# Kernel optimization log

Hardware: AMD Instinct MI355X
Metric: run time of the kernel (lower is better)

## Reference

```python
import jax, jax.numpy as jnp
import numpy as np

B, P, D = 8, 576, 1024
H = 16
HD = D // H  # 64
HID = 4 * D  # 4096
EPS = 1e-6  # flax LayerNorm default


def _ln(x, g, b):
    m = jnp.mean(x, axis=-1, keepdims=True)
    v = jnp.var(x, axis=-1, keepdims=True)
    return (x - m) * jax.lax.rsqrt(v + EPS) * g + b


def setup_inputs() -> dict:
    key = jax.random.key(0)
    ks = jax.random.split(key, 8)
    s = 0.02
    return {
        "x": jax.random.normal(ks[0], (B, P, D), dtype=jnp.float32),
        "w_qkv": jax.random.normal(ks[1], (D, 3 * D), dtype=jnp.float32) * s,
        "q_g": jnp.ones((HD,), jnp.float32), "q_b": jnp.zeros((HD,), jnp.float32),
        "k_g": jnp.ones((HD,), jnp.float32), "k_b": jnp.zeros((HD,), jnp.float32),
        "o_g": jnp.ones((D,), jnp.float32), "o_b": jnp.zeros((D,), jnp.float32),
        "w_proj": jax.random.normal(ks[2], (D, D), dtype=jnp.float32) * s,
        "b_proj": jnp.zeros((D,), jnp.float32),
        "ln1_g": jnp.ones((D,), jnp.float32), "ln1_b": jnp.zeros((D,), jnp.float32),
        "ln2_g": jnp.ones((D,), jnp.float32), "ln2_b": jnp.zeros((D,), jnp.float32),
        "w1": jax.random.normal(ks[3], (D, HID), dtype=jnp.float32) * s,
        "b1": jnp.zeros((HID,), jnp.float32),
        "w2": jax.random.normal(ks[4], (HID, D), dtype=jnp.float32) * s,
        "b2": jnp.zeros((D,), jnp.float32),
        "ls1": jnp.full((D,), 1e-5, jnp.float32),
        "ls2": jnp.full((D,), 1e-5, jnp.float32),
    }


def reference(x, w_qkv, q_g, q_b, k_g, k_b, o_g, o_b, w_proj, b_proj,
              ln1_g, ln1_b, ln2_g, ln2_b, w1, b1, w2, b2, ls1, ls2):
    scale = HD ** (-0.5)
    # --- attention branch ---
    o = _ln(x, ln1_g, ln1_b)
    qkv = jnp.einsum('bpd,de->bpe', o, w_qkv)
    qkv = qkv.reshape(B, P, 3, H, HD).transpose(2, 0, 3, 1, 4)  # [3,B,H,P,HD]
    q, k, v = qkv[0], qkv[1], qkv[2]
    q = _ln(q, q_g, q_b) * scale  # QK-LayerNorm per head
    k = _ln(k, k_g, k_b)
    attn = jax.nn.softmax(jnp.einsum('bhqd,bhkd->bhqk', q, k), axis=-1)
    o = jnp.einsum('bhqk,bhkd->bhqd', attn, v)
    o = jnp.swapaxes(o, 1, 2).reshape(B, P, D)
    o = _ln(o, o_g, o_b)
    o = jnp.einsum('bpd,de->bpe', o, w_proj) + b_proj
    x = x + o * ls1
    # --- MLP branch ---
    o = _ln(x, ln2_g, ln2_b)
    o = jax.nn.gelu(jnp.einsum('bpd,dh->bph', o, w1) + b1)  # tanh-approx gelu (flax default)
    o = jnp.einsum('bph,hd->bpd', o, w2) + b2
    return x + o * ls2
```

## Files before the change

kernel.cpp:

```cpp
#include <hip/hip_runtime.h>
#include <hip/hip_bf16.h>

#define DEV static __device__ __forceinline__

typedef short frag8 __attribute__((ext_vector_type(8)));
typedef float accf4 __attribute__((ext_vector_type(4)));


DEV unsigned short f2bf(float f){
  union { float f; unsigned int u; } v; v.f = f;
  unsigned int r = v.u + 0x7fffu + ((v.u >> 16) & 1u);
  return (unsigned short)(r >> 16);
}

DEV void gload16(const void* g, void* l){
  __builtin_amdgcn_global_load_lds((const __attribute__((address_space(1))) void*)g,
                                   (__attribute__((address_space(3))) void*)l, 16, 0, 0);
}

DEV float gelu_tanh(float x){
  float u = 0.7978845608028654f * (x + 0.044715f * x * x * x);
  float e = __expf(2.0f * u);
  float th = 1.0f - 2.0f / (e + 1.0f);
  return 0.5f * x * (1.0f + th);
}

DEV void block_map(int bid, int nwg, int gx, int& tx, int& ty){
  const int swz = ((nwg & 7) == 0) ? ((bid & 7) * (nwg >> 3) + (bid >> 3)) : bid;
  const int gy = nwg / gx;
  const int cg = swz / (gy * 16);
  const int rr = swz - cg * gy * 16;
  const int gw = min(16, gx - cg * 16);
  tx = cg * 16 + rr % gw;
  ty = rr / gw;
}

__global__ __launch_bounds__(256) void wtrans(const float* __restrict__ W,
                                              unsigned short* __restrict__ Wt,
                                              int K, int N){
  __shared__ float t[32][33];
  const int n0 = blockIdx.x * 32, k0 = blockIdx.y * 32;
  const int tx = threadIdx.x, ty = threadIdx.y;
  #pragma unroll
  for (int i = 0; i < 4; i++)
    t[ty + i*8][tx] = W[(long)(k0 + ty + i*8) * N + n0 + tx];
  __syncthreads();
  #pragma unroll
  for (int i = 0; i < 4; i++)
    Wt[(long)(n0 + ty + i*8) * K + k0 + tx] = f2bf(t[tx][ty + i*8]);
}

__global__ __launch_bounds__(256) void ln_rows(const float* __restrict__ in,
                                               const float* __restrict__ g,
                                               const float* __restrict__ beta,
                                               unsigned short* __restrict__ out){
  const long row = blockIdx.x;
  const int t = threadIdx.x;
  const float4 v = ((const float4*)(in + row * 1024))[t];
  float s  = v.x + v.y + v.z + v.w;
  float s2 = v.x*v.x + v.y*v.y + v.z*v.z + v.w*v.w;
  #pragma unroll
  for (int o = 32; o; o >>= 1){ s += __shfl_xor(s, o); s2 += __shfl_xor(s2, o); }
  __shared__ float rs[4], rq[4];
  const int wv = t >> 6;
  if ((t & 63) == 0){ rs[wv] = s; rq[wv] = s2; }
  __syncthreads();
  s  = rs[0] + rs[1] + rs[2] + rs[3];
  s2 = rq[0] + rq[1] + rq[2] + rq[3];
  const float mean = s * (1.f/1024.f);
  const float inv = rsqrtf(s2 * (1.f/1024.f) - mean*mean + 1e-6f);
  const float4 gv = ((const float4*)g)[t];
  const float4 bv = ((const float4*)beta)[t];
  ushort4 o4;
  o4.x = f2bf((v.x - mean)*inv*gv.x + bv.x);
  o4.y = f2bf((v.y - mean)*inv*gv.y + bv.y);
  o4.z = f2bf((v.z - mean)*inv*gv.z + bv.z);
  o4.w = f2bf((v.w - mean)*inv*gv.w + bv.w);
  *(ushort4*)(out + row * 1024 + t * 4) = o4;
}

__global__ __launch_bounds__(256) void attn_k(const unsigned short* __restrict__ Qn,
                                              const unsigned short* __restrict__ Kn,
                                              const unsigned short* __restrict__ Vt,
                                              float* __restrict__ O){
  __shared__ __align__(16) unsigned short Ks[2][4096];
  __shared__ __align__(16) unsigned short Vs[2][4096];
  __shared__ __align__(16) unsigned short Plds[4096];
  const int f = blockIdx.x;
  const int xcd = f & 7, j = f >> 3;
  const int bh = xcd * 16 + j / 9;
  const int qb = j - (j / 9) * 9;
  const int b = bh >> 4, h = bh & 15;
  const int tid = threadIdx.x, w = tid >> 6, l = tid & 63;
  const int fr = l & 15, fq = l >> 4;
  const int rsw = fr & 7;
  const int q0 = qb * 64;

  const unsigned short* qbase = Qn + ((long)bh * 576 + q0 + w * 16 + fr) * 64;
  const frag8 qf0 = *(const frag8*)(qbase + fq * 8);
  const frag8 qf1 = *(const frag8*)(qbase + 32 + fq * 8);

  const int r8 = l >> 3;
  const int kq8 = ((l & 7) ^ r8) * 8;
  const unsigned short* kSrc = Kn + ((long)bh * 576 + w * 16 + r8) * 64 + kq8;
  const unsigned short* vSrc = Vt + ((long)bh * 64 + w * 16 + r8) * 576 + kq8;

  auto stage = [&](int d, int t){
    gload16(kSrc + (long)t * 4096,              &Ks[d][w * 1024]);
    gload16(kSrc + (long)t * 4096 + 512,        &Ks[d][w * 1024 + 512]);
    gload16(vSrc + (long)t * 64,                &Vs[d][w * 1024]);
    gload16(vSrc + (long)t * 64 + 8l * 576,     &Vs[d][w * 1024 + 512]);
  };

  accf4 oacc[4];
  #pragma unroll
  for (int nd = 0; nd < 4; nd++) oacc[nd] = (accf4){0.f, 0.f, 0.f, 0.f};
  float m[4] = {-1e30f, -1e30f, -1e30f, -1e30f};
  float lsum[4] = {0.f, 0.f, 0.f, 0.f};

  stage(0, 0);
  __syncthreads();
  int cur = 0;
  for (int t = 0; t < 9; ++t){
    if (t < 8) stage(cur ^ 1, t + 1);

    accf4 st[4];
    #pragma unroll
    for (int kt4 = 0; kt4 < 4; kt4++){
      const int c0 = ((0 * 4 + fq) ^ rsw) * 8;
      const int c1 = ((1 * 4 + fq) ^ rsw) * 8;
      frag8 kf0 = *(const frag8*)&Ks[cur][(kt4 * 16 + fr) * 64 + c0];
      frag8 kf1 = *(const frag8*)&Ks[cur][(kt4 * 16 + fr) * 64 + c1];
      accf4 a = {0.f, 0.f, 0.f, 0.f};
      a = __builtin_amdgcn_mfma_f32_16x16x32_bf16(qf0, kf0, a, 0, 0, 0);
      a = __builtin_amdgcn_mfma_f32_16x16x32_bf16(qf1, kf1, a, 0, 0, 0);
      st[kt4] = a;
    }

    #pragma unroll
    for (int rr = 0; rr < 4; rr++){
      float v = fmaxf(fmaxf(st[0][rr], st[1][rr]), fmaxf(st[2][rr], st[3][rr]));
      #pragma unroll
      for (int o = 8; o; o >>= 1) v = fmaxf(v, __shfl_xor(v, o));
      const float mn = fmaxf(m[rr], v);
      const float sc = __expf(m[rr] - mn);
      float p[4], rs = 0.f;
      #pragma unroll
      for (int kt4 = 0; kt4 < 4; kt4++){ p[kt4] = __expf(st[kt4][rr] - mn); rs += p[kt4]; }
      #pragma unroll
      for (int o = 8; o; o >>= 1) rs += __shfl_xor(rs, o);
      lsum[rr] = lsum[rr] * sc + rs;
      m[rr] = mn;
      #pragma unroll
      for (int nd = 0; nd < 4; nd++) oacc[nd][rr] *= sc;
      const int prow = fq * 4 + rr;
      #pragma unroll
      for (int kt4 = 0; kt4 < 4; kt4++){
        const int chunk = kt4 * 2 + (fr >> 3);
        Plds[w * 1024 + prow * 64 + ((chunk ^ (prow & 7)) << 3) + (fr & 7)] = f2bf(p[kt4]);
      }
    }

    #pragma unroll
    for (int nd = 0; nd < 4; nd++){
      const int c0 = ((0 * 4 + fq) ^ rsw) * 8;
      const int c1 = ((1 * 4 + fq) ^ rsw) * 8;
      frag8 af0 = *(const frag8*)&Plds[w * 1024 + fr * 64 + c0];
      frag8 af1 = *(const frag8*)&Plds[w * 1024 + fr * 64 + c1];
      frag8 vf0 = *(const frag8*)&Vs[cur][(nd * 16 + fr) * 64 + c0];
      frag8 vf1 = *(const frag8*)&Vs[cur][(nd * 16 + fr) * 64 + c1];
      oacc[nd] = __builtin_amdgcn_mfma_f32_16x16x32_bf16(af0, vf0, oacc[nd], 0, 0, 0);
      oacc[nd] = __builtin_amdgcn_mfma_f32_16x16x32_bf16(af1, vf1, oacc[nd], 0, 0, 0);
    }

    __syncthreads();
    cur ^= 1;
  }

  #pragma unroll
  for (int rr = 0; rr < 4; rr++){
    const float rinv = 1.f / lsum[rr];
    const long orow = (long)b * 576 + q0 + w * 16 + fq * 4 + rr;
    #pragma unroll
    for (int nd = 0; nd < 4; nd++)
      O[orow * 1024 + h * 64 + nd * 16 + fr] = oacc[nd][rr] * rinv;
  }
}

template<int BN, int EPI>
__global__ __launch_bounds__(256) void gemm_bk64(
    const unsigned short* __restrict__ A, const unsigned short* __restrict__ Bt,
    float* __restrict__ Cf, unsigned short* __restrict__ Cb,
    const float* __restrict__ bias, const float* __restrict__ ls,
    const float* __restrict__ resid,
    const float* __restrict__ qg, const float* __restrict__ qb2,
    const float* __restrict__ kg, const float* __restrict__ kb2,
    unsigned short* __restrict__ Qn, unsigned short* __restrict__ Kn,
    unsigned short* __restrict__ Vt,
    int M, int N, int K, int gx)
{
  constexpr int NF = BN / 32;
  constexpr int BSLOT = BN / 32;
  __shared__ __align__(16) unsigned short As[2][128 * 64];
  __shared__ __align__(16) unsigned short Bs[2][BN * 64];
  const int tid = threadIdx.x;
  const int wave = tid >> 6, l = tid & 63;
  const int fr = l & 15, fq = l >> 4;
  const int wr = wave >> 1, wc = wave & 1;
  const int rsw = fr & 7;
  int tx, ty;
  block_map(blockIdx.x, gridDim.x, gx, tx, ty);
  const long rowbase = (long)ty * 128;
  const long colbase = (long)tx * BN;

  const int r8 = l >> 3;
  const int kq = (l & 7) ^ r8;
  const unsigned short* aS = A + (rowbase + wave*32 + r8) * (long)K + kq * 8;
  const unsigned short* bS = Bt + (colbase + wave*(BN/4) + r8) * (long)K + kq * 8;

  accf4 acc[4][NF];
  const accf4 zero = {0.f, 0.f, 0.f, 0.f};
  #pragma unroll
  for (int m = 0; m < 4; m++)
    #pragma unroll
    for (int n = 0; n < NF; n++) acc[m][n] = zero;

  auto stage = [&](int d, int t){
    const long k0 = (long)t * 64;
    #pragma unroll
    for (int s = 0; s < 4; s++)
      gload16(aS + (long)s * 8 * K + k0, &As[d][(wave*4 + s) * 512]);
    #pragma unroll
    for (int s = 0; s < BSLOT; s++)
      gload16(bS + (long)s * 8 * K + k0, &Bs[d][(wave*BSLOT + s) * 512]);
  };
  auto compute = [&](int d){
    #pragma unroll
    for (int kk = 0; kk < 2; kk++){
      const int csw = ((kk * 4 + fq) ^ rsw) * 8;
      frag8 bf[NF];
      #pragma unroll
      for (int n = 0; n < NF; n++)
        bf[n] = *(const frag8*)&Bs[d][(wc*(BN/2) + n*16 + fr) * 64 + csw];
      #pragma unroll
      for (int m = 0; m < 4; m++){
        frag8 af = *(const frag8*)&As[d][(wr*64 + m*16 + fr) * 64 + csw];
        #pragma unroll
        for (int n = 0; n < NF; n++)
          acc[m][n] = __builtin_amdgcn_mfma_f32_16x16x32_bf16(af, bf[n], acc[m][n], 0, 0, 0);
      }
    }
  };

  const int NT = K >> 6;
  stage(0, 0);
  __syncthreads();
  int cur = 0;
  for (int t = 0; t < NT; ++t){
    if (t + 1 < NT) stage(cur ^ 1, t + 1);
    compute(cur);
    __syncthreads();
    cur ^= 1;
  }

  if constexpr (EPI == 3){
    const int cg = (int)colbase + wc * 64;
    const int kind = cg >> 10;
    const int h = (cg & 1023) >> 6;
    if (kind < 2){
      const float* g  = kind ? kg : qg;
      const float* bb = kind ? kb2 : qb2;
      const float sc = kind ? 1.0f : 0.125f;
      unsigned short* Out = kind ? Kn : Qn;
      #pragma unroll
      for (int m = 0; m < 4; m++){
        #pragma unroll
        for (int r = 0; r < 4; r++){
          float s1 = 0.f, s2 = 0.f;
          #pragma unroll
          for (int n = 0; n < NF; n++){ const float v = acc[m][n][r]; s1 += v; s2 += v*v; }
          #pragma unroll
          for (int o = 8; o; o >>= 1){ s1 += __shfl_xor(s1, o); s2 += __shfl_xor(s2, o); }
          const float mean = s1 * (1.f/64.f);
          const float inv = rsqrtf(s2 * (1.f/64.f) - mean*mean + 1e-6f);
          const long row = rowbase + wr*64 + m*16 + fq*4 + r;
          const int bq = (int)(row / 576), p = (int)(row - (long)bq*576);
          unsigned short* dst = Out + (((long)(bq*16 + h))*576 + p)*64;
          #pragma unroll
          for (int n = 0; n < NF; n++){
            const int d = n*16 + fr;
            dst[d] = f2bf(((acc[m][n][r] - mean)*inv*g[d] + bb[d]) * sc);
          }
        }
      }
    } else {
      #pragma unroll
      for (int m = 0; m < 4; m++){
        const long grow = rowbase + wr*64 + m*16 + fq*4;
        const int bq = (int)(grow / 576), p = (int)(grow - (long)bq*576);
        #pragma unroll
        for (int n = 0; n < NF; n++){
          const int d = n*16 + fr;
          ushort4 o4;
          o4.x = f2bf(acc[m][n][0]); o4.y = f2bf(acc[m][n][1]);
          o4.z = f2bf(acc[m][n][2]); o4.w = f2bf(acc[m][n][3]);
          *(ushort4*)(Vt + ((long)(bq*16 + h)*64 + d)*576 + p) = o4;
        }
      }
    }
  } else {
    #pragma unroll
    for (int m = 0; m < 4; m++){
      const long rb = rowbase + wr * 64 + m * 16 + fq * 4;
      #pragma unroll
      for (int n = 0; n < NF; n++){
        const long cb = colbase + wc * (BN/2) + n * 16 + fr;
        #pragma unroll
        for (int r = 0; r < 4; r++){
          const long idx = (rb + r) * N + cb;
          const float v = acc[m][n][r];
          if constexpr (EPI == 1){
            Cf[idx] = resid[idx] + (v + bias[cb]) * ls[cb];
          } else {
            Cb[idx] = f2bf(gelu_tanh(v + bias[cb]));
          }
        }
      }
    }
  }
}

extern "C" void kernel_launch(void* const* d_in, const int* in_sizes, int n_in,
                              void* d_out, int out_size, void* d_ws, size_t ws_size,
                              hipStream_t stream){
  (void)in_sizes; (void)n_in; (void)out_size; (void)ws_size;
  const float* x      = (const float*)d_in[0];
  const float* w_qkv  = (const float*)d_in[1];
  const float* q_g    = (const float*)d_in[2];
  const float* q_b    = (const float*)d_in[3];
  const float* k_g    = (const float*)d_in[4];
  const float* k_b    = (const float*)d_in[5];
  const float* o_g    = (const float*)d_in[6];
  const float* o_b    = (const float*)d_in[7];
  const float* w_proj = (const float*)d_in[8];
  const float* b_proj = (const float*)d_in[9];
  const float* ln1_g  = (const float*)d_in[10];
  const float* ln1_b  = (const float*)d_in[11];
  const float* ln2_g  = (const float*)d_in[12];
  const float* ln2_b  = (const float*)d_in[13];
  const float* w1     = (const float*)d_in[14];
  const float* b1     = (const float*)d_in[15];
  const float* w2     = (const float*)d_in[16];
  const float* b2     = (const float*)d_in[17];
  const float* ls1    = (const float*)d_in[18];
  const float* ls2    = (const float*)d_in[19];
  float* out = (float*)d_out;

  char* ws = (char*)d_ws;
  size_t off = 0;
  auto alloc = [&](size_t bytes)->void*{
    void* p = ws + off; off += (bytes + 255) & ~(size_t)255; return p;
  };
  unsigned short* wqkvT  = (unsigned short*)alloc(3072l*1024*2);
  unsigned short* wprojT = (unsigned short*)alloc(1024l*1024*2);
  unsigned short* w1T    = (unsigned short*)alloc(4096l*1024*2);
  unsigned short* w2T    = (unsigned short*)alloc(1024l*4096*2);
  unsigned short* xnA    = (unsigned short*)alloc(4608l*1024*2);
  unsigned short* Qn     = (unsigned short*)alloc(73728l*64*2);
  unsigned short* Kn     = (unsigned short*)alloc(73728l*64*2);
  unsigned short* Vt     = (unsigned short*)alloc(73728l*64*2);
  unsigned short* hbf    = (unsigned short*)alloc(4608l*4096*2);
  float*          attnO  = (float*)alloc(4608l*1024*4);

  wtrans<<<dim3(3072/32, 1024/32), dim3(32,8), 0, stream>>>(w_qkv,  wqkvT,  1024, 3072);
  wtrans<<<dim3(1024/32, 1024/32), dim3(32,8), 0, stream>>>(w_proj, wprojT, 1024, 1024);
  wtrans<<<dim3(4096/32, 1024/32), dim3(32,8), 0, stream>>>(w1,     w1T,    1024, 4096);
  wtrans<<<dim3(1024/32, 4096/32), dim3(32,8), 0, stream>>>(w2,     w2T,    4096, 1024);

  ln_rows<<<4608, 256, 0, stream>>>(x, ln1_g, ln1_b, xnA);
  gemm_bk64<128,3><<<24*36, 256, 0, stream>>>(xnA, wqkvT, nullptr, nullptr,
                                              nullptr, nullptr, nullptr,
                                              q_g, q_b, k_g, k_b, Qn, Kn, Vt,
                                              4608, 3072, 1024, 24);
  attn_k<<<1152, 256, 0, stream>>>(Qn, Kn, Vt, attnO);
  ln_rows<<<4608, 256, 0, stream>>>(attnO, o_g, o_b, xnA);
  gemm_bk64<64,1><<<16*36, 256, 0, stream>>>(xnA, wprojT, out, nullptr,
                                             b_proj, ls1, x,
                                             nullptr, nullptr, nullptr, nullptr,
                                             nullptr, nullptr, nullptr,
                                             4608, 1024, 1024, 16);
  ln_rows<<<4608, 256, 0, stream>>>(out, ln2_g, ln2_b, xnA);
  gemm_bk64<64,2><<<64*36, 256, 0, stream>>>(xnA, w1T, nullptr, hbf,
                                             b1, nullptr, nullptr,
                                             nullptr, nullptr, nullptr, nullptr,
                                             nullptr, nullptr, nullptr,
                                             4608, 4096, 1024, 64);
  gemm_bk64<64,1><<<16*36, 256, 0, stream>>>(hbf, w2T, out, nullptr,
                                             b2, ls2, out,
                                             nullptr, nullptr, nullptr, nullptr,
                                             nullptr, nullptr, nullptr,
                                             4608, 1024, 4096, 16);
}
```

Before: 266.0 us.

## Store attention output in bf16 and split QKV GEMM into QK and V launches

The attention kernel now writes its output as bf16 instead of fp32, and the following LayerNorm reads bf16 through a templated loader, halving that intermediate's traffic. The fused QKV GEMM is split into a Q/K GEMM with the per-head LayerNorm epilogue and a separate V GEMM with BN=64 that writes the transposed V layout. This removes the divergent epilogue branch but adds a kernel launch and reloads the A operand. Rounding the attention output to bf16 before LayerNorm adds a small loss of precision.

```diff
diff --git a/kernel.cpp b/kernel.cpp
--- a/kernel.cpp
+++ b/kernel.cpp
@@ -11,6 +11,10 @@
   union { float f; unsigned int u; } v; v.f = f;
   unsigned int r = v.u + 0x7fffu + ((v.u >> 16) & 1u);
   return (unsigned short)(r >> 16);
+}
+
+DEV float bf2f(unsigned short u){
+  union { unsigned int i; float f; } v; v.i = (unsigned int)u << 16; return v.f;
 }
 
 DEV void gload16(const void* g, void* l){
@@ -50,13 +54,20 @@
     Wt[(long)(n0 + ty + i*8) * K + k0 + tx] = f2bf(t[tx][ty + i*8]);
 }
 
-__global__ __launch_bounds__(256) void ln_rows(const float* __restrict__ in,
+template<int BF>
+__global__ __launch_bounds__(256) void ln_rows(const void* __restrict__ inp,
                                                const float* __restrict__ g,
                                                const float* __restrict__ beta,
                                                unsigned short* __restrict__ out){
   const long row = blockIdx.x;
   const int t = threadIdx.x;
-  const float4 v = ((const float4*)(in + row * 1024))[t];
+  float4 v;
+  if constexpr (BF){
+    const ushort4 u = ((const ushort4*)inp)[row * 256 + t];
+    v.x = bf2f(u.x); v.y = bf2f(u.y); v.z = bf2f(u.z); v.w = bf2f(u.w);
+  } else {
+    v = ((const float4*)inp)[row * 256 + t];
+  }
   float s  = v.x + v.y + v.z + v.w;
   float s2 = v.x*v.x + v.y*v.y + v.z*v.z + v.w*v.w;
   #pragma unroll
@@ -82,7 +93,7 @@
 __global__ __launch_bounds__(256) void attn_k(const unsigned short* __restrict__ Qn,
                                               const unsigned short* __restrict__ Kn,
                                               const unsigned short* __restrict__ Vt,
-                                              float* __restrict__ O){
+                                              unsigned short* __restrict__ O){
   __shared__ __align__(16) unsigned short Ks[2][4096];
   __shared__ __align__(16) unsigned short Vs[2][4096];
   __shared__ __align__(16) unsigned short Plds[4096];
@@ -183,7 +194,7 @@
     const long orow = (long)b * 576 + q0 + w * 16 + fq * 4 + rr;
     #pragma unroll
     for (int nd = 0; nd < 4; nd++)
-      O[orow * 1024 + h * 64 + nd * 16 + fr] = oacc[nd][rr] * rinv;
+      O[orow * 1024 + h * 64 + nd * 16 + fr] = f2bf(oacc[nd][rr] * rinv);
   }
 }
 
@@ -267,45 +278,44 @@
     const int cg = (int)colbase + wc * 64;
     const int kind = cg >> 10;
     const int h = (cg & 1023) >> 6;
-    if (kind < 2){
-      const float* g  = kind ? kg : qg;
-      const float* bb = kind ? kb2 : qb2;
-      const float sc = kind ? 1.0f : 0.125f;
-      unsigned short* Out = kind ? Kn : Qn;
-      #pragma unroll
-      for (int m = 0; m < 4; m++){
+    const float* g  = kind ? kg : qg;
+    const float* bb = kind ? kb2 : qb2;
+    const float sc = kind ? 1.0f : 0.125f;
+    unsigned short* Out = kind ? Kn : Qn;
+    #pragma unroll
+    for (int m = 0; m < 4; m++){
+      #pragma unroll
+      for (int r = 0; r < 4; r++){
+        float s1 = 0.f, s2 = 0.f;
         #pragma unroll
-        for (int r = 0; r < 4; r++){
-          float s1 = 0.f, s2 = 0.f;
-          #pragma unroll
-          for (int n = 0; n < NF; n++){ const float v = acc[m][n][r]; s1 += v; s2 += v*v; }
-          #pragma unroll
-          for (int o = 8; o; o >>= 1){ s1 += __shfl_xor(s1, o); s2 += __shfl_xor(s2, o); }
-          const float mean = s1 * (1.f/64.f);
-          const float inv = rsqrtf(s2 * (1.f/64.f) - mean*mean + 1e-6f);
-          const long row = rowbase + wr*64 + m*16 + fq*4 + r;
-          const int bq = (int)(row / 576), p = (int)(row - (long)bq*576);
-          unsigned short* dst = Out + (((long)(bq*16 + h))*576 + p)*64;
-          #pragma unroll
-          for (int n = 0; n < NF; n++){
-            const int d = n*16 + fr;
-            dst[d] = f2bf(((acc[m][n][r] - mean)*inv*g[d] + bb[d]) * sc);
-          }
-        }
-      }
-    } else {
-      #pragma unroll
-      for (int m = 0; m < 4; m++){
-        const long grow = rowbase + wr*64 + m*16 + fq*4;
-        const int bq = (int)(grow / 576), p = (int)(grow - (long)bq*576);
+        for (int n = 0; n < NF; n++){ const float v = acc[m][n][r]; s1 += v; s2 += v*v; }
+        #pragma unroll
+        for (int o = 8; o; o >>= 1){ s1 += __shfl_xor(s1, o); s2 += __shfl_xor(s2, o); }
+        const float mean = s1 * (1.f/64.f);
+        const float inv = rsqrtf(s2 * (1.f/64.f) - mean*mean + 1e-6f);
+        const long row = rowbase + wr*64 + m*16 + fq*4 + r;
+        const int bq = (int)(row / 576), p = (int)(row - (long)bq*576);
+        unsigned short* dst = Out + (((long)(bq*16 + h))*576 + p)*64;
         #pragma unroll
         for (int n = 0; n < NF; n++){
           const int d = n*16 + fr;
-          ushort4 o4;
-          o4.x = f2bf(acc[m][n][0]); o4.y = f2bf(acc[m][n][1]);
-          o4.z = f2bf(acc[m][n][2]); o4.w = f2bf(acc[m][n][3]);
-          *(ushort4*)(Vt + ((long)(bq*16 + h)*64 + d)*576 + p) = o4;
+          dst[d] = f2bf(((acc[m][n][r] - mean)*inv*g[d] + bb[d]) * sc);
         }
+      }
+    }
+  } else if constexpr (EPI == 4){
+    const int h = (int)colbase >> 6;
+    #pragma unroll
+    for (int m = 0; m < 4; m++){
+      const long grow = rowbase + wr*64 + m*16 + fq*4;
+      const int bq = (int)(grow / 576), p = (int)(grow - (long)bq*576);
+      #pragma unroll
+      for (int n = 0; n < NF; n++){
+        const int d = wc*(BN/2) + n*16 + fr;
+        ushort4 o4;
+        o4.x = f2bf(acc[m][n][0]); o4.y = f2bf(acc[m][n][1]);
+        o4.z = f2bf(acc[m][n][2]); o4.w = f2bf(acc[m][n][3]);
+        *(ushort4*)(Vt + ((long)(bq*16 + h)*64 + d)*576 + p) = o4;
       }
     }
   } else {
@@ -370,26 +380,31 @@
   unsigned short* Kn     = (unsigned short*)alloc(73728l*64*2);
   unsigned short* Vt     = (unsigned short*)alloc(73728l*64*2);
   unsigned short* hbf    = (unsigned short*)alloc(4608l*4096*2);
-  float*          attnO  = (float*)alloc(4608l*1024*4);
+  unsigned short* attnO  = (unsigned short*)alloc(4608l*1024*2);
 
   wtrans<<<dim3(3072/32, 1024/32), dim3(32,8), 0, stream>>>(w_qkv,  wqkvT,  1024, 3072);
   wtrans<<<dim3(1024/32, 1024/32), dim3(32,8), 0, stream>>>(w_proj, wprojT, 1024, 1024);
   wtrans<<<dim3(4096/32, 1024/32), dim3(32,8), 0, stream>>>(w1,     w1T,    1024, 4096);
   wtrans<<<dim3(1024/32, 4096/32), dim3(32,8), 0, stream>>>(w2,     w2T,    4096, 1024);
 
-  ln_rows<<<4608, 256, 0, stream>>>(x, ln1_g, ln1_b, xnA);
-  gemm_bk64<128,3><<<24*36, 256, 0, stream>>>(xnA, wqkvT, nullptr, nullptr,
+  ln_rows<0><<<4608, 256, 0, stream>>>(x, ln1_g, ln1_b, xnA);
+  gemm_bk64<128,3><<<16*36, 256, 0, stream>>>(xnA, wqkvT, nullptr, nullptr,
                                               nullptr, nullptr, nullptr,
-                                              q_g, q_b, k_g, k_b, Qn, Kn, Vt,
-                                              4608, 3072, 1024, 24);
+                                              q_g, q_b, k_g, k_b, Qn, Kn, nullptr,
+                                              4608, 2048, 1024, 16);
+  gemm_bk64<64,4><<<16*36, 256, 0, stream>>>(xnA, wqkvT + 2048l*1024, nullptr, nullptr,
+                                             nullptr, nullptr, nullptr,
+                                             nullptr, nullptr, nullptr, nullptr,
+                                             nullptr, nullptr, Vt,
+                                             4608, 1024, 1024, 16);
   attn_k<<<1152, 256, 0, stream>>>(Qn, Kn, Vt, attnO);
-  ln_rows<<<4608, 256, 0, stream>>>(attnO, o_g, o_b, xnA);
+  ln_rows<1><<<4608, 256, 0, stream>>>(attnO, o_g, o_b, xnA);
   gemm_bk64<64,1><<<16*36, 256, 0, stream>>>(xnA, wprojT, out, nullptr,
                                              b_proj, ls1, x,
                                              nullptr, nullptr, nullptr, nullptr,
                                              nullptr, nullptr, nullptr,
                                              4608, 1024, 1024, 16);
-  ln_rows<<<4608, 256, 0, stream>>>(out, ln2_g, ln2_b, xnA);
+  ln_rows<0><<<4608, 256, 0, stream>>>(out, ln2_g, ln2_b, xnA);
   gemm_bk64<64,2><<<64*36, 256, 0, stream>>>(xnA, w1T, nullptr, hbf,
                                              b1, nullptr, nullptr,
                                              nullptr, nullptr, nullptr, nullptr,
```

Measured after the change: 272.5 us. 1.02x slower.
